# Optimization experiments

Hardware: AMD Instinct MI355X
Metric: run time of the kernel (lower is better)

Reference implementation:

```python
import jax, jax.numpy as jnp
import numpy as np

EMBED_DIM = 768
N_HEADS = 12
HEAD_DIM = EMBED_DIM // N_HEADS
B, T = 2, 4096


def setup_inputs() -> dict:
    key = jax.random.key(0)
    k1, k2, k3, k4, k5 = jax.random.split(key, 5)
    s = 1.0 / np.sqrt(EMBED_DIM)
    return {
        "x": jax.random.normal(k1, (B, T, EMBED_DIM), dtype=jnp.float32),
        "Wqkv": jax.random.normal(k2, (EMBED_DIM, 3 * EMBED_DIM), dtype=jnp.float32) * s,
        "bqkv": jnp.zeros((3 * EMBED_DIM,), dtype=jnp.float32),
        "Wproj": jax.random.normal(k3, (EMBED_DIM, EMBED_DIM), dtype=jnp.float32) * s,
        "bproj": jnp.zeros((EMBED_DIM,), dtype=jnp.float32),
    }


def reference(x, Wqkv, bqkv, Wproj, bproj):
    Bz, Tz, C = x.shape
    qkv = x @ Wqkv + bqkv                         # [B,T,3C]
    q, k, v = jnp.split(qkv, 3, axis=2)
    # [B,T,H,D] -> [B,H,T,D]
    def heads(t):
        return t.reshape(Bz, Tz, N_HEADS, HEAD_DIM).transpose(0, 2, 1, 3)
    q, k, v = heads(q), heads(k), heads(v)
    scale = 1.0 / np.sqrt(HEAD_DIM)
    att = jnp.einsum("bhqd,bhkd->bhqk", q, k) * scale   # [B,H,T,T]
    causal = jnp.tril(jnp.ones((Tz, Tz), dtype=bool))
    att = jnp.where(causal[None, None], att, -jnp.inf)
    att = jax.nn.softmax(att, axis=-1)
    y = jnp.einsum("bhqk,bhkd->bhqd", att, v)            # [B,H,T,D]
    y = y.transpose(0, 2, 1, 3).reshape(Bz, Tz, C)
    return y @ Wproj + bproj
```

## Files before the change

### kernel.cpp

```cpp
#include <hip/hip_runtime.h>
#include <math.h>
#include <stdint.h>

typedef __attribute__((ext_vector_type(8))) short bf16x8;
typedef __attribute__((ext_vector_type(4))) float f32x4;

__device__ __forceinline__ unsigned short f2bf(float f) {
    union { float f; unsigned u; } v; v.f = f;
    return (unsigned short)((v.u + 0x7fffu + ((v.u >> 16) & 1u)) >> 16);
}

__device__ __forceinline__ void gld_lds16(const void* g, void* l) {
    __builtin_amdgcn_global_load_lds(
        (const __attribute__((address_space(1))) unsigned*)(uintptr_t)g,
        (__attribute__((address_space(3))) unsigned*)(uintptr_t)l, 16, 0, 0);
}

__global__ void k_convert(const float* __restrict__ in, unsigned short* __restrict__ out, int n4) {
    int i = blockIdx.x * blockDim.x + threadIdx.x;
    if (i >= n4) return;
    float4 f = ((const float4*)in)[i];
    ushort4 o;
    o.x = f2bf(f.x); o.y = f2bf(f.y); o.z = f2bf(f.z); o.w = f2bf(f.w);
    ((ushort4*)out)[i] = o;
}

__global__ void k_transpose(const float* __restrict__ in, unsigned short* __restrict__ out, int R, int C) {
    __shared__ float tile[32][33];
    int c0 = blockIdx.x * 32, r0 = blockIdx.y * 32;
    int tx = threadIdx.x, ty = threadIdx.y;
#pragma unroll
    for (int i = 0; i < 4; ++i)
        tile[ty + i * 8][tx] = in[(size_t)(r0 + ty + i * 8) * C + c0 + tx];
    __syncthreads();
#pragma unroll
    for (int i = 0; i < 4; ++i)
        out[(size_t)(c0 + ty + i * 8) * R + r0 + tx] = f2bf(tile[tx][ty + i * 8]);
}

#define LDT 32

__device__ __forceinline__ void gemm_core(
    const unsigned short* __restrict__ A, const unsigned short* __restrict__ Bt,
    int K, unsigned short* As, unsigned short* Bs, f32x4 (&acc)[4][4])
{
    const int tid  = threadIdx.x;
    const int lane = tid & 63;
    const int w    = tid >> 6;
    const int wm   = (w >> 1) * 64, wn = (w & 1) * 64;
    const int l15  = lane & 15, quad = lane >> 4;
    const int m0 = blockIdx.x * 128, n0 = blockIdx.y * 128;

    const f32x4 zero = {0.f, 0.f, 0.f, 0.f};
#pragma unroll
    for (int i = 0; i < 4; ++i)
#pragma unroll
        for (int j = 0; j < 4; ++j) acc[i][j] = zero;

    const int r0 = tid >> 2, p8 = (tid & 3) * 8;
    const unsigned short* Ag0 = A  + (size_t)(m0 + r0) * K + p8;
    const unsigned short* Ag1 = A  + (size_t)(m0 + r0 + 64) * K + p8;
    const unsigned short* Bg0 = Bt + (size_t)(n0 + r0) * K + p8;
    const unsigned short* Bg1 = Bt + (size_t)(n0 + r0 + 64) * K + p8;
    unsigned short* lA0 = As + r0 * LDT + p8;
    unsigned short* lA1 = lA0 + 64 * LDT;
    unsigned short* lB0 = Bs + r0 * LDT + p8;
    unsigned short* lB1 = lB0 + 64 * LDT;

    const int nk = K >> 5;
    for (int kt = 0; kt < nk; ++kt) {
        __syncthreads();
        gld_lds16(Ag0, lA0);
        gld_lds16(Ag1, lA1);
        gld_lds16(Bg0, lB0);
        gld_lds16(Bg1, lB1);
        Ag0 += 32; Ag1 += 32; Bg0 += 32; Bg1 += 32;
        __syncthreads();
        bf16x8 af[4], bfr[4];
#pragma unroll
        for (int mi = 0; mi < 4; ++mi)
            af[mi] = *(const bf16x8*)&As[(wm + mi * 16 + l15) * LDT + quad * 8];
#pragma unroll
        for (int nj = 0; nj < 4; ++nj)
            bfr[nj] = *(const bf16x8*)&Bs[(wn + nj * 16 + l15) * LDT + quad * 8];
#pragma unroll
        for (int mi = 0; mi < 4; ++mi)
#pragma unroll
            for (int nj = 0; nj < 4; ++nj)
                acc[mi][nj] = __builtin_amdgcn_mfma_f32_16x16x32_bf16(af[mi], bfr[nj], acc[mi][nj], 0, 0, 0);
    }
}

__global__ __launch_bounds__(256) void k_gemm_qkv(
    const unsigned short* __restrict__ A, const unsigned short* __restrict__ Bt,
    const float* __restrict__ bias,
    unsigned short* __restrict__ QL, unsigned short* __restrict__ KL,
    unsigned short* __restrict__ VL)
{
    __shared__ __align__(16) unsigned short As[128 * LDT];
    __shared__ __align__(16) unsigned short Bs[128 * LDT];
    f32x4 acc[4][4];
    gemm_core(A, Bt, 768, As, Bs, acc);

    const int tid = threadIdx.x, lane = tid & 63, w = tid >> 6;
    const int wm = (w >> 1) * 64, wn = (w & 1) * 64;
    const int l15 = lane & 15, quad = lane >> 4;
    const int m0 = blockIdx.x * 128, n0 = blockIdx.y * 128;
    const float cscale = 0.18033688011f;
#pragma unroll
    for (int nj = 0; nj < 4; ++nj) {
        int cg = n0 + wn + nj * 16 + l15;
        float bv = bias[cg];
        int which = cg / 768;
        int rem = cg - which * 768;
        int hd = rem >> 6, d = rem & 63;
        float sc = (which == 0) ? cscale : 1.0f;
#pragma unroll
        for (int mi = 0; mi < 4; ++mi) {
#pragma unroll
            for (int r = 0; r < 4; ++r) {
                int rg = m0 + wm + mi * 16 + quad * 4 + r;
                int b = rg >> 12, tk = rg & 4095;
                int bh = b * 12 + hd;
                unsigned short ob = f2bf((acc[mi][nj][r] + bv) * sc);
                if (which == 0) {
                    size_t idx = ((((size_t)bh * 128 + (tk >> 5)) * 2 + ((tk >> 4) & 1)) * 2 + (d >> 5)) * 512
                               + ((d >> 3) & 3) * 128 + (tk & 15) * 8 + (d & 7);
                    QL[idx] = ob;
                } else if (which == 1) {
                    size_t idx = ((((size_t)bh * 64 + (tk >> 6)) * 4 + ((tk >> 4) & 3)) * 2 + (d >> 5)) * 512
                               + ((d >> 3) & 3) * 128 + (tk & 15) * 8 + (d & 7);
                    KL[idx] = ob;
                } else {
                    int wi = tk & 63;
                    size_t idx = ((((size_t)bh * 64 + (tk >> 6)) * 4 + (d >> 4)) * 2 + (wi >> 5)) * 512
                               + ((wi >> 3) & 3) * 128 + (d & 15) * 8 + (wi & 7);
                    VL[idx] = ob;
                }
            }
        }
    }
}

__global__ __launch_bounds__(256) void k_gemm_proj(
    const unsigned short* __restrict__ A, const unsigned short* __restrict__ Bt,
    const float* __restrict__ bias, float* __restrict__ out)
{
    __shared__ __align__(16) unsigned short As[128 * LDT];
    __shared__ __align__(16) unsigned short Bs[128 * LDT];
    f32x4 acc[4][4];
    gemm_core(A, Bt, 768, As, Bs, acc);

    const int tid = threadIdx.x, lane = tid & 63, w = tid >> 6;
    const int wm = (w >> 1) * 64, wn = (w & 1) * 64;
    const int l15 = lane & 15, quad = lane >> 4;
    const int m0 = blockIdx.x * 128, n0 = blockIdx.y * 128;
#pragma unroll
    for (int nj = 0; nj < 4; ++nj) {
        int cg = n0 + wn + nj * 16 + l15;
        float bv = bias[cg];
#pragma unroll
        for (int mi = 0; mi < 4; ++mi)
#pragma unroll
            for (int r = 0; r < 4; ++r) {
                int rg = m0 + wm + mi * 16 + quad * 4 + r;
                out[(size_t)rg * 768 + cg] = acc[mi][nj][r] + bv;
            }
    }
}

#define LDP 68

__global__ __launch_bounds__(128) void k_attn(
    const unsigned short* __restrict__ QL, const unsigned short* __restrict__ KL,
    const unsigned short* __restrict__ VL, unsigned short* __restrict__ Y)
{
    __shared__ __align__(16) char smem[17408];
    unsigned short* Ps = (unsigned short*)smem;

    const int tid = threadIdx.x, lane = tid & 63;
    const int w = __builtin_amdgcn_readfirstlane(tid >> 6);
    const int l15 = lane & 15, quad = lane >> 4;
    const int id = blockIdx.x;
    const int bh = id % 24;
    const int g  = 63 - id / 24;
    const int qi = 2 * g + w;
    const int q0 = qi * 32;
    const int nkt = g + 1;
    unsigned short* Pw = Ps + w * 2 * 32 * LDP;

    const int pw_off = l15 * LDP + quad * 4;
    const int pr_off = l15 * LDP + quad * 8;

    const unsigned short* Qb = QL + (((size_t)bh * 128 + qi) * 4) * 512 + lane * 8;
    const unsigned short* kp = KL + ((size_t)bh * 64) * 4096 + lane * 8;
    const unsigned short* vp = VL + ((size_t)bh * 64) * 4096 + lane * 8;

    bf16x8 qt[2][2];
#pragma unroll
    for (int m = 0; m < 2; ++m)
#pragma unroll
        for (int h = 0; h < 2; ++h)
            qt[m][h] = *(const bf16x8*)(Qb + (m * 2 + h) * 512);

    const f32x4 zero = {0.f, 0.f, 0.f, 0.f};
    f32x4 O[2][4], lac[2];
#pragma unroll
    for (int m = 0; m < 2; ++m) {
        lac[m] = zero;
#pragma unroll
        for (int dj = 0; dj < 4; ++dj) O[m][dj] = zero;
    }

    const short ONE = (short)0x3F80;
    const bf16x8 onesf = {ONE, ONE, ONE, ONE, ONE, ONE, ONE, ONE};

    bf16x8 ka[4][2], vf[4][2];
#pragma unroll
    for (int i = 0; i < 4; ++i)
#pragma unroll
        for (int h = 0; h < 2; ++h)
            ka[i][h] = *(const bf16x8*)(kp + (i * 2 + h) * 512);
#pragma unroll
    for (int dj = 0; dj < 4; ++dj)
#pragma unroll
        for (int h = 0; h < 2; ++h)
            vf[dj][h] = *(const bf16x8*)(vp + (dj * 2 + h) * 512);

    {
        f32x4 st[2][4];
#pragma unroll
        for (int i = 0; i < 4; ++i)
#pragma unroll
            for (int m = 0; m < 2; ++m) {
                f32x4 z = __builtin_amdgcn_mfma_f32_16x16x32_bf16(ka[i][0], qt[m][0], zero, 0, 0, 0);
                st[m][i] = __builtin_amdgcn_mfma_f32_16x16x32_bf16(ka[i][1], qt[m][1], z, 0, 0, 0);
            }
        if (nkt == 1) {
#pragma unroll
            for (int m = 0; m < 2; ++m)
#pragma unroll
                for (int i = 0; i < 4; ++i)
#pragma unroll
                    for (int r = 0; r < 4; ++r)
                        if (i * 16 + quad * 4 + r > q0 + m * 16 + l15)
                            st[m][i][r] = -INFINITY;
        }
#pragma unroll
        for (int m = 0; m < 2; ++m)
#pragma unroll
            for (int i = 0; i < 4; ++i) {
                unsigned e0 = __float_as_uint(__builtin_amdgcn_exp2f(st[m][i][0])) + 0x8000u;
                unsigned e1 = __float_as_uint(__builtin_amdgcn_exp2f(st[m][i][1])) + 0x8000u;
                unsigned e2 = __float_as_uint(__builtin_amdgcn_exp2f(st[m][i][2])) + 0x8000u;
                unsigned e3 = __float_as_uint(__builtin_amdgcn_exp2f(st[m][i][3])) + 0x8000u;
                uint2 pk;
                pk.x = __builtin_amdgcn_perm(e1, e0, 0x07060302);
                pk.y = __builtin_amdgcn_perm(e3, e2, 0x07060302);
                *(uint2*)(Pw + pw_off + m * 16 * LDP + i * 16) = pk;
            }
    }

    for (int kt = 0; kt < nkt; ++kt) {
        unsigned short* bc = Pw + (kt & 1) * 32 * LDP;
        unsigned short* bn = Pw + ((kt & 1) ^ 1) * 32 * LDP;
        const bool more = (kt + 1 < nkt);

        bf16x8 pa[2][2];
#pragma unroll
        for (int m = 0; m < 2; ++m) {
            pa[m][0] = *(const bf16x8*)(bc + pr_off + m * 16 * LDP);
            pa[m][1] = *(const bf16x8*)(bc + pr_off + m * 16 * LDP + 32);
        }

        if (more) {
            kp += 4096;
#pragma unroll
            for (int i = 0; i < 4; ++i)
#pragma unroll
                for (int h = 0; h < 2; ++h)
                    ka[i][h] = *(const bf16x8*)(kp + (i * 2 + h) * 512);
        }

        __builtin_amdgcn_s_setprio(1);
#pragma unroll
        for (int m = 0; m < 2; ++m) {
            f32x4 z = __builtin_amdgcn_mfma_f32_16x16x32_bf16(pa[m][0], onesf, lac[m], 0, 0, 0);
            lac[m] = __builtin_amdgcn_mfma_f32_16x16x32_bf16(pa[m][1], onesf, z, 0, 0, 0);
        }
#pragma unroll
        for (int dj = 0; dj < 4; ++dj)
#pragma unroll
            for (int m = 0; m < 2; ++m) {
                f32x4 z = __builtin_amdgcn_mfma_f32_16x16x32_bf16(pa[m][0], vf[dj][0], O[m][dj], 0, 0, 0);
                O[m][dj] = __builtin_amdgcn_mfma_f32_16x16x32_bf16(pa[m][1], vf[dj][1], z, 0, 0, 0);
            }
        __builtin_amdgcn_s_setprio(0);

        if (more) {
            vp += 4096;
#pragma unroll
            for (int dj = 0; dj < 4; ++dj)
#pragma unroll
                for (int h = 0; h < 2; ++h)
                    vf[dj][h] = *(const bf16x8*)(vp + (dj * 2 + h) * 512);

            __builtin_amdgcn_s_setprio(1);
            f32x4 st[2][4];
#pragma unroll
            for (int i = 0; i < 4; ++i)
#pragma unroll
                for (int m = 0; m < 2; ++m) {
                    f32x4 z = __builtin_amdgcn_mfma_f32_16x16x32_bf16(ka[i][0], qt[m][0], zero, 0, 0, 0);
                    st[m][i] = __builtin_amdgcn_mfma_f32_16x16x32_bf16(ka[i][1], qt[m][1], z, 0, 0, 0);
                }
            __builtin_amdgcn_s_setprio(0);
            if (kt + 1 == nkt - 1) {
                const int kb = (kt + 1) * 64;
#pragma unroll
                for (int m = 0; m < 2; ++m)
#pragma unroll
                    for (int i = 0; i < 4; ++i)
#pragma unroll
                        for (int r = 0; r < 4; ++r)
                            if (kb + i * 16 + quad * 4 + r > q0 + m * 16 + l15)
                                st[m][i][r] = -INFINITY;
            }
#pragma unroll
            for (int m = 0; m < 2; ++m)
#pragma unroll
                for (int i = 0; i < 4; ++i) {
                    unsigned e0 = __float_as_uint(__builtin_amdgcn_exp2f(st[m][i][0])) + 0x8000u;
                    unsigned e1 = __float_as_uint(__builtin_amdgcn_exp2f(st[m][i][1])) + 0x8000u;
                    unsigned e2 = __float_as_uint(__builtin_amdgcn_exp2f(st[m][i][2])) + 0x8000u;
                    unsigned e3 = __float_as_uint(__builtin_amdgcn_exp2f(st[m][i][3])) + 0x8000u;
                    uint2 pk;
                    pk.x = __builtin_amdgcn_perm(e1, e0, 0x07060302);
                    pk.y = __builtin_amdgcn_perm(e3, e2, 0x07060302);
                    *(uint2*)(bn + pw_off + m * 16 * LDP + i * 16) = pk;
                }
        }
    }

    const int b = bh / 12, hd = bh % 12;
#pragma unroll
    for (int m = 0; m < 2; ++m)
#pragma unroll
        for (int r = 0; r < 4; ++r) {
            float inv = 1.0f / lac[m][r];
            int t = q0 + 16 * m + quad * 4 + r;
            size_t base = ((size_t)(b * 4096 + t)) * 768 + hd * 64;
#pragma unroll
            for (int dj = 0; dj < 4; ++dj)
                Y[base + dj * 16 + l15] = f2bf(O[m][dj][r] * inv);
        }
}

extern "C" void kernel_launch(void* const* d_in, const int* in_sizes, int n_in,
                              void* d_out, int out_size, void* d_ws, size_t ws_size,
                              hipStream_t stream) {
    (void)in_sizes; (void)n_in; (void)out_size; (void)ws_size;
    const float* x     = (const float*)d_in[0];
    const float* Wqkv  = (const float*)d_in[1];
    const float* bqkv  = (const float*)d_in[2];
    const float* Wproj = (const float*)d_in[3];
    const float* bproj = (const float*)d_in[4];
    float* out = (float*)d_out;

    char* ws = (char*)d_ws;
    size_t off = 0;
    auto alloc = [&](size_t bytes) -> void* {
        void* p = ws + off;
        off += (bytes + 255) & ~(size_t)255;
        return p;
    };
    unsigned short* xb     = (unsigned short*)alloc((size_t)8192 * 768 * 2);
    unsigned short* WqkvT  = (unsigned short*)alloc((size_t)2304 * 768 * 2);
    unsigned short* WprojT = (unsigned short*)alloc((size_t)768 * 768 * 2);
    unsigned short* QLb    = (unsigned short*)alloc((size_t)24 * 4096 * 64 * 2);
    unsigned short* KLb    = (unsigned short*)alloc((size_t)24 * 4096 * 64 * 2);
    unsigned short* VLb    = (unsigned short*)alloc((size_t)24 * 4096 * 64 * 2);
    unsigned short* Yb     = (unsigned short*)alloc((size_t)8192 * 768 * 2);

    k_convert<<<6144, 256, 0, stream>>>(x, xb, 8192 * 768 / 4);
    dim3 tb(32, 8);
    k_transpose<<<dim3(72, 24), tb, 0, stream>>>(Wqkv, WqkvT, 768, 2304);
    k_transpose<<<dim3(24, 24), tb, 0, stream>>>(Wproj, WprojT, 768, 768);
    k_gemm_qkv<<<dim3(64, 18), 256, 0, stream>>>(xb, WqkvT, bqkv, QLb, KLb, VLb);
    k_attn<<<dim3(1536), 128, 0, stream>>>(QLb, KLb, VLb, Yb);
    k_gemm_proj<<<dim3(64, 6), 256, 0, stream>>>(Yb, WprojT, bproj, out);
}
```

Before: 246.2 us.

## Process 64 query rows per single-wave attention block to reuse K/V fragments

The attention kernel changes from two waves of 32 query rows each to one wave covering all 64 query rows of the block. Each K/V fragment loaded from global memory is now reused across four 16-row query tiles instead of two, which halves redundant K/V loads per query. In exchange, blocks are 64 threads with doubled accumulator and Q register state per wave, so register pressure rises and fewer waves are available to hide latency. The S and P work is also interleaved per 16-row group.

```diff
diff --git a/kernel.cpp b/kernel.cpp
--- a/kernel.cpp
+++ b/kernel.cpp
@@ -171,42 +171,38 @@
 
 #define LDP 68
 
-__global__ __launch_bounds__(128) void k_attn(
+__global__ __launch_bounds__(64) void k_attn(
     const unsigned short* __restrict__ QL, const unsigned short* __restrict__ KL,
     const unsigned short* __restrict__ VL, unsigned short* __restrict__ Y)
 {
-    __shared__ __align__(16) char smem[17408];
-    unsigned short* Ps = (unsigned short*)smem;
-
-    const int tid = threadIdx.x, lane = tid & 63;
-    const int w = __builtin_amdgcn_readfirstlane(tid >> 6);
+    __shared__ __align__(16) unsigned short Ps[2 * 64 * LDP];
+
+    const int lane = threadIdx.x & 63;
     const int l15 = lane & 15, quad = lane >> 4;
     const int id = blockIdx.x;
     const int bh = id % 24;
     const int g  = 63 - id / 24;
-    const int qi = 2 * g + w;
-    const int q0 = qi * 32;
+    const int q0 = g * 64;
     const int nkt = g + 1;
-    unsigned short* Pw = Ps + w * 2 * 32 * LDP;
 
     const int pw_off = l15 * LDP + quad * 4;
     const int pr_off = l15 * LDP + quad * 8;
 
-    const unsigned short* Qb = QL + (((size_t)bh * 128 + qi) * 4) * 512 + lane * 8;
+    const unsigned short* Qb = QL + (((size_t)bh * 128 + 2 * g) * 4) * 512 + lane * 8;
     const unsigned short* kp = KL + ((size_t)bh * 64) * 4096 + lane * 8;
     const unsigned short* vp = VL + ((size_t)bh * 64) * 4096 + lane * 8;
 
-    bf16x8 qt[2][2];
-#pragma unroll
-    for (int m = 0; m < 2; ++m)
+    bf16x8 qt[4][2];
+#pragma unroll
+    for (int m = 0; m < 4; ++m)
 #pragma unroll
         for (int h = 0; h < 2; ++h)
-            qt[m][h] = *(const bf16x8*)(Qb + (m * 2 + h) * 512);
+            qt[m][h] = *(const bf16x8*)(Qb + ((m >> 1) * 4 + (m & 1) * 2 + h) * 512);
 
     const f32x4 zero = {0.f, 0.f, 0.f, 0.f};
-    f32x4 O[2][4], lac[2];
-#pragma unroll
-    for (int m = 0; m < 2; ++m) {
+    f32x4 O[4][4], lac[4];
+#pragma unroll
+    for (int m = 0; m < 4; ++m) {
         lac[m] = zero;
 #pragma unroll
         for (int dj = 0; dj < 4; ++dj) O[m][dj] = zero;
@@ -227,51 +223,39 @@
         for (int h = 0; h < 2; ++h)
             vf[dj][h] = *(const bf16x8*)(vp + (dj * 2 + h) * 512);
 
-    {
-        f32x4 st[2][4];
-#pragma unroll
-        for (int i = 0; i < 4; ++i)
-#pragma unroll
-            for (int m = 0; m < 2; ++m) {
-                f32x4 z = __builtin_amdgcn_mfma_f32_16x16x32_bf16(ka[i][0], qt[m][0], zero, 0, 0, 0);
-                st[m][i] = __builtin_amdgcn_mfma_f32_16x16x32_bf16(ka[i][1], qt[m][1], z, 0, 0, 0);
-            }
+#pragma unroll
+    for (int m = 0; m < 4; ++m) {
+        f32x4 st[4];
+#pragma unroll
+        for (int i = 0; i < 4; ++i) {
+            f32x4 z = __builtin_amdgcn_mfma_f32_16x16x32_bf16(ka[i][0], qt[m][0], zero, 0, 0, 0);
+            st[i] = __builtin_amdgcn_mfma_f32_16x16x32_bf16(ka[i][1], qt[m][1], z, 0, 0, 0);
+        }
         if (nkt == 1) {
 #pragma unroll
-            for (int m = 0; m < 2; ++m)
-#pragma unroll
-                for (int i = 0; i < 4; ++i)
-#pragma unroll
-                    for (int r = 0; r < 4; ++r)
-                        if (i * 16 + quad * 4 + r > q0 + m * 16 + l15)
-                            st[m][i][r] = -INFINITY;
-        }
-#pragma unroll
-        for (int m = 0; m < 2; ++m)
-#pragma unroll
-            for (int i = 0; i < 4; ++i) {
-                unsigned e0 = __float_as_uint(__builtin_amdgcn_exp2f(st[m][i][0])) + 0x8000u;
-                unsigned e1 = __float_as_uint(__builtin_amdgcn_exp2f(st[m][i][1])) + 0x8000u;
-                unsigned e2 = __float_as_uint(__builtin_amdgcn_exp2f(st[m][i][2])) + 0x8000u;
-                unsigned e3 = __float_as_uint(__builtin_amdgcn_exp2f(st[m][i][3])) + 0x8000u;
-                uint2 pk;
-                pk.x = __builtin_amdgcn_perm(e1, e0, 0x07060302);
-                pk.y = __builtin_amdgcn_perm(e3, e2, 0x07060302);
-                *(uint2*)(Pw + pw_off + m * 16 * LDP + i * 16) = pk;
-            }
+            for (int i = 0; i < 4; ++i)
+#pragma unroll
+                for (int r = 0; r < 4; ++r)
+                    if (i * 16 + quad * 4 + r > q0 + m * 16 + l15)
+                        st[i][r] = -INFINITY;
+        }
+#pragma unroll
+        for (int i = 0; i < 4; ++i) {
+            unsigned e0 = __float_as_uint(__builtin_amdgcn_exp2f(st[i][0])) + 0x8000u;
+            unsigned e1 = __float_as_uint(__builtin_amdgcn_exp2f(st[i][1])) + 0x8000u;
+            unsigned e2 = __float_as_uint(__builtin_amdgcn_exp2f(st[i][2])) + 0x8000u;
+            unsigned e3 = __float_as_uint(__builtin_amdgcn_exp2f(st[i][3])) + 0x8000u;
+            uint2 pk;
+            pk.x = __builtin_amdgcn_perm(e1, e0, 0x07060302);
+            pk.y = __builtin_amdgcn_perm(e3, e2, 0x07060302);
+            *(uint2*)(Ps + pw_off + m * 16 * LDP + i * 16) = pk;
+        }
     }
 
     for (int kt = 0; kt < nkt; ++kt) {
-        unsigned short* bc = Pw + (kt & 1) * 32 * LDP;
-        unsigned short* bn = Pw + ((kt & 1) ^ 1) * 32 * LDP;
+        unsigned short* bc = Ps + (kt & 1) * 64 * LDP;
+        unsigned short* bn = Ps + ((kt & 1) ^ 1) * 64 * LDP;
         const bool more = (kt + 1 < nkt);
-
-        bf16x8 pa[2][2];
-#pragma unroll
-        for (int m = 0; m < 2; ++m) {
-            pa[m][0] = *(const bf16x8*)(bc + pr_off + m * 16 * LDP);
-            pa[m][1] = *(const bf16x8*)(bc + pr_off + m * 16 * LDP + 32);
-        }
 
         if (more) {
             kp += 4096;
@@ -284,17 +268,17 @@
 
         __builtin_amdgcn_s_setprio(1);
 #pragma unroll
-        for (int m = 0; m < 2; ++m) {
-            f32x4 z = __builtin_amdgcn_mfma_f32_16x16x32_bf16(pa[m][0], onesf, lac[m], 0, 0, 0);
-            lac[m] = __builtin_amdgcn_mfma_f32_16x16x32_bf16(pa[m][1], onesf, z, 0, 0, 0);
-        }
-#pragma unroll
-        for (int dj = 0; dj < 4; ++dj)
-#pragma unroll
-            for (int m = 0; m < 2; ++m) {
-                f32x4 z = __builtin_amdgcn_mfma_f32_16x16x32_bf16(pa[m][0], vf[dj][0], O[m][dj], 0, 0, 0);
-                O[m][dj] = __builtin_amdgcn_mfma_f32_16x16x32_bf16(pa[m][1], vf[dj][1], z, 0, 0, 0);
+        for (int m = 0; m < 4; ++m) {
+            bf16x8 pa0 = *(const bf16x8*)(bc + pr_off + m * 16 * LDP);
+            bf16x8 pa1 = *(const bf16x8*)(bc + pr_off + m * 16 * LDP + 32);
+            f32x4 z = __builtin_amdgcn_mfma_f32_16x16x32_bf16(pa0, onesf, lac[m], 0, 0, 0);
+            lac[m] = __builtin_amdgcn_mfma_f32_16x16x32_bf16(pa1, onesf, z, 0, 0, 0);
+#pragma unroll
+            for (int dj = 0; dj < 4; ++dj) {
+                f32x4 y = __builtin_amdgcn_mfma_f32_16x16x32_bf16(pa0, vf[dj][0], O[m][dj], 0, 0, 0);
+                O[m][dj] = __builtin_amdgcn_mfma_f32_16x16x32_bf16(pa1, vf[dj][1], y, 0, 0, 0);
             }
+        }
         __builtin_amdgcn_s_setprio(0);
 
         if (more) {
@@ -305,46 +289,44 @@
                 for (int h = 0; h < 2; ++h)
                     vf[dj][h] = *(const bf16x8*)(vp + (dj * 2 + h) * 512);
 
-            __builtin_amdgcn_s_setprio(1);
-            f32x4 st[2][4];
-#pragma unroll
-            for (int i = 0; i < 4; ++i)
-#pragma unroll
-                for (int m = 0; m < 2; ++m) {
+            const int kb = (kt + 1) * 64;
+            const bool diag = (kt + 1 == nkt - 1);
+#pragma unroll
+            for (int m = 0; m < 4; ++m) {
+                __builtin_amdgcn_s_setprio(1);
+                f32x4 st[4];
+#pragma unroll
+                for (int i = 0; i < 4; ++i) {
                     f32x4 z = __builtin_amdgcn_mfma_f32_16x16x32_bf16(ka[i][0], qt[m][0], zero, 0, 0, 0);
-                    st[m][i] = __builtin_amdgcn_mfma_f32_16x16x32_bf16(ka[i][1], qt[m][1], z, 0, 0, 0);
+                    st[i] = __builtin_amdgcn_mfma_f32_16x16x32_bf16(ka[i][1], qt[m][1], z, 0, 0, 0);
                 }
-            __builtin_amdgcn_s_setprio(0);
-            if (kt + 1 == nkt - 1) {
-                const int kb = (kt + 1) * 64;
-#pragma unroll
-                for (int m = 0; m < 2; ++m)
+                __builtin_amdgcn_s_setprio(0);
+                if (diag) {
 #pragma unroll
                     for (int i = 0; i < 4; ++i)
 #pragma unroll
                         for (int r = 0; r < 4; ++r)
                             if (kb + i * 16 + quad * 4 + r > q0 + m * 16 + l15)
-                                st[m][i][r] = -INFINITY;
-            }
-#pragma unroll
-            for (int m = 0; m < 2; ++m)
+                                st[i][r] = -INFINITY;
+                }
 #pragma unroll
                 for (int i = 0; i < 4; ++i) {
-                    unsigned e0 = __float_as_uint(__builtin_amdgcn_exp2f(st[m][i][0])) + 0x8000u;
-                    unsigned e1 = __float_as_uint(__builtin_amdgcn_exp2f(st[m][i][1])) + 0x8000u;
-                    unsigned e2 = __float_as_uint(__builtin_amdgcn_exp2f(st[m][i][2])) + 0x8000u;
-                    unsigned e3 = __float_as_uint(__builtin_amdgcn_exp2f(st[m][i][3])) + 0x8000u;
+                    unsigned e0 = __float_as_uint(__builtin_amdgcn_exp2f(st[i][0])) + 0x8000u;
+                    unsigned e1 = __float_as_uint(__builtin_amdgcn_exp2f(st[i][1])) + 0x8000u;
+                    unsigned e2 = __float_as_uint(__builtin_amdgcn_exp2f(st[i][2])) + 0x8000u;
+                    unsigned e3 = __float_as_uint(__builtin_amdgcn_exp2f(st[i][3])) + 0x8000u;
                     uint2 pk;
                     pk.x = __builtin_amdgcn_perm(e1, e0, 0x07060302);
                     pk.y = __builtin_amdgcn_perm(e3, e2, 0x07060302);
                     *(uint2*)(bn + pw_off + m * 16 * LDP + i * 16) = pk;
                 }
+            }
         }
     }
 
     const int b = bh / 12, hd = bh % 12;
 #pragma unroll
-    for (int m = 0; m < 2; ++m)
+    for (int m = 0; m < 4; ++m)
 #pragma unroll
         for (int r = 0; r < 4; ++r) {
             float inv = 1.0f / lac[m][r];
@@ -387,6 +369,6 @@
     k_transpose<<<dim3(72, 24), tb, 0, stream>>>(Wqkv, WqkvT, 768, 2304);
     k_transpose<<<dim3(24, 24), tb, 0, stream>>>(Wproj, WprojT, 768, 768);
     k_gemm_qkv<<<dim3(64, 18), 256, 0, stream>>>(xb, WqkvT, bqkv, QLb, KLb, VLb);
-    k_attn<<<dim3(1536), 128, 0, stream>>>(QLb, KLb, VLb, Yb);
+    k_attn<<<dim3(1536), 64, 0, stream>>>(QLb, KLb, VLb, Yb);
     k_gemm_proj<<<dim3(64, 6), 256, 0, stream>>>(Yb, WprojT, bproj, out);
 }
```

Result: slower. 282.9 us (+14.9%).

## Share K/V tiles across four waves via LDS with async global-to-LDS prefetch

Applied to the files above, without the earlier changes.

The attention kernel now runs 4 waves per block, each handling one 32-row query tile. K and V tiles are staged once per block into double-buffered LDS with global_load_lds prefetch, replacing the per-wave direct global loads into registers. Each wave stops at its own causal diagonal, while the block-wide loop runs to the longest wave's length and syncs every iteration. This cuts redundant global/L2 traffic for K/V at the cost of a barrier per tile, idle waves on the shorter query tiles, and larger LDS use per block.

```diff
diff --git a/kernel.cpp b/kernel.cpp
--- a/kernel.cpp
+++ b/kernel.cpp
@@ -171,30 +171,33 @@
 
 #define LDP 68
 
-__global__ __launch_bounds__(128) void k_attn(
+__global__ __launch_bounds__(256) void k_attn(
     const unsigned short* __restrict__ QL, const unsigned short* __restrict__ KL,
     const unsigned short* __restrict__ VL, unsigned short* __restrict__ Y)
 {
-    __shared__ __align__(16) char smem[17408];
-    unsigned short* Ps = (unsigned short*)smem;
+    __shared__ __align__(16) unsigned short Kb[2 * 4096];
+    __shared__ __align__(16) unsigned short Vb[2 * 4096];
+    __shared__ __align__(16) unsigned short Ps[4 * 2 * 32 * LDP];
 
     const int tid = threadIdx.x, lane = tid & 63;
     const int w = __builtin_amdgcn_readfirstlane(tid >> 6);
     const int l15 = lane & 15, quad = lane >> 4;
     const int id = blockIdx.x;
     const int bh = id % 24;
-    const int g  = 63 - id / 24;
-    const int qi = 2 * g + w;
+    const int gi = 31 - id / 24;
+    const int qi = 4 * gi + w;
     const int q0 = qi * 32;
-    const int nkt = g + 1;
-    unsigned short* Pw = Ps + w * 2 * 32 * LDP;
+    const int nkt = 2 * gi + 2;
+    const int ktd = qi >> 1;
+    const int nw  = ktd + 1;
+    unsigned short* Pw = Ps + w * (2 * 32 * LDP);
 
     const int pw_off = l15 * LDP + quad * 4;
     const int pr_off = l15 * LDP + quad * 8;
 
     const unsigned short* Qb = QL + (((size_t)bh * 128 + qi) * 4) * 512 + lane * 8;
-    const unsigned short* kp = KL + ((size_t)bh * 64) * 4096 + lane * 8;
-    const unsigned short* vp = VL + ((size_t)bh * 64) * 4096 + lane * 8;
+    const unsigned short* Kg = KL + ((size_t)bh * 64) * 4096;
+    const unsigned short* Vg = VL + ((size_t)bh * 64) * 4096;
 
     bf16x8 qt[2][2];
 #pragma unroll
@@ -211,23 +214,26 @@
 #pragma unroll
         for (int dj = 0; dj < 4; ++dj) O[m][dj] = zero;
     }
-
     const short ONE = (short)0x3F80;
     const bf16x8 onesf = {ONE, ONE, ONE, ONE, ONE, ONE, ONE, ONE};
 
-    bf16x8 ka[4][2], vf[4][2];
-#pragma unroll
-    for (int i = 0; i < 4; ++i)
-#pragma unroll
-        for (int h = 0; h < 2; ++h)
-            ka[i][h] = *(const bf16x8*)(kp + (i * 2 + h) * 512);
-#pragma unroll
-    for (int dj = 0; dj < 4; ++dj)
-#pragma unroll
-        for (int h = 0; h < 2; ++h)
-            vf[dj][h] = *(const bf16x8*)(vp + (dj * 2 + h) * 512);
+    gld_lds16(Kg + tid * 8,            Kb + tid * 8);
+    gld_lds16(Kg + 2048 + tid * 8,     Kb + 2048 + tid * 8);
+    gld_lds16(Kg + 4096 + tid * 8,     Kb + 4096 + tid * 8);
+    gld_lds16(Kg + 6144 + tid * 8,     Kb + 6144 + tid * 8);
+    gld_lds16(Vg + tid * 8,            Vb + tid * 8);
+    gld_lds16(Vg + 2048 + tid * 8,     Vb + 2048 + tid * 8);
+    __syncthreads();
 
     {
+        bf16x8 ka[4][2];
+#pragma unroll
+        for (int i = 0; i < 4; ++i)
+#pragma unroll
+            for (int h = 0; h < 2; ++h)
+                ka[i][h] = *(const bf16x8*)(Kb + (i * 2 + h) * 512 + lane * 8);
+        __syncthreads();
+
         f32x4 st[2][4];
 #pragma unroll
         for (int i = 0; i < 4; ++i)
@@ -236,7 +242,7 @@
                 f32x4 z = __builtin_amdgcn_mfma_f32_16x16x32_bf16(ka[i][0], qt[m][0], zero, 0, 0, 0);
                 st[m][i] = __builtin_amdgcn_mfma_f32_16x16x32_bf16(ka[i][1], qt[m][1], z, 0, 0, 0);
             }
-        if (nkt == 1) {
+        if (ktd == 0) {
 #pragma unroll
             for (int m = 0; m < 2; ++m)
 #pragma unroll
@@ -262,48 +268,59 @@
     }
 
     for (int kt = 0; kt < nkt; ++kt) {
-        unsigned short* bc = Pw + (kt & 1) * 32 * LDP;
-        unsigned short* bn = Pw + ((kt & 1) ^ 1) * 32 * LDP;
-        const bool more = (kt + 1 < nkt);
-
-        bf16x8 pa[2][2];
-#pragma unroll
-        for (int m = 0; m < 2; ++m) {
-            pa[m][0] = *(const bf16x8*)(bc + pr_off + m * 16 * LDP);
-            pa[m][1] = *(const bf16x8*)(bc + pr_off + m * 16 * LDP + 32);
-        }
-
-        if (more) {
-            kp += 4096;
+        const int cur = kt & 1;
+
+        if (kt + 2 < nkt) {
+            const unsigned short* s = Kg + (size_t)(kt + 2) * 4096;
+            unsigned short* d = Kb + cur * 4096;
+            gld_lds16(s + tid * 8, d + tid * 8);
+            gld_lds16(s + 2048 + tid * 8, d + 2048 + tid * 8);
+        }
+        if (kt + 1 < nkt) {
+            const unsigned short* s = Vg + (size_t)(kt + 1) * 4096;
+            unsigned short* d = Vb + (cur ^ 1) * 4096;
+            gld_lds16(s + tid * 8, d + tid * 8);
+            gld_lds16(s + 2048 + tid * 8, d + 2048 + tid * 8);
+        }
+
+        if (kt < nw) {
+            const unsigned short* bc = Pw + cur * 32 * LDP;
+            bf16x8 pa[2][2];
+#pragma unroll
+            for (int m = 0; m < 2; ++m) {
+                pa[m][0] = *(const bf16x8*)(bc + pr_off + m * 16 * LDP);
+                pa[m][1] = *(const bf16x8*)(bc + pr_off + m * 16 * LDP + 32);
+            }
+            bf16x8 vf[4][2];
+#pragma unroll
+            for (int dj = 0; dj < 4; ++dj)
+#pragma unroll
+                for (int h = 0; h < 2; ++h)
+                    vf[dj][h] = *(const bf16x8*)(Vb + cur * 4096 + (dj * 2 + h) * 512 + lane * 8);
+
+            __builtin_amdgcn_s_setprio(1);
+#pragma unroll
+            for (int m = 0; m < 2; ++m) {
+                f32x4 z = __builtin_amdgcn_mfma_f32_16x16x32_bf16(pa[m][0], onesf, lac[m], 0, 0, 0);
+                lac[m] = __builtin_amdgcn_mfma_f32_16x16x32_bf16(pa[m][1], onesf, z, 0, 0, 0);
+            }
+#pragma unroll
+            for (int dj = 0; dj < 4; ++dj)
+#pragma unroll
+                for (int m = 0; m < 2; ++m) {
+                    f32x4 y = __builtin_amdgcn_mfma_f32_16x16x32_bf16(pa[m][0], vf[dj][0], O[m][dj], 0, 0, 0);
+                    O[m][dj] = __builtin_amdgcn_mfma_f32_16x16x32_bf16(pa[m][1], vf[dj][1], y, 0, 0, 0);
+                }
+            __builtin_amdgcn_s_setprio(0);
+        }
+
+        if (kt + 1 < nw) {
+            bf16x8 ka[4][2];
 #pragma unroll
             for (int i = 0; i < 4; ++i)
 #pragma unroll
                 for (int h = 0; h < 2; ++h)
-                    ka[i][h] = *(const bf16x8*)(kp + (i * 2 + h) * 512);
-        }
-
-        __builtin_amdgcn_s_setprio(1);
-#pragma unroll
-        for (int m = 0; m < 2; ++m) {
-            f32x4 z = __builtin_amdgcn_mfma_f32_16x16x32_bf16(pa[m][0], onesf, lac[m], 0, 0, 0);
-            lac[m] = __builtin_amdgcn_mfma_f32_16x16x32_bf16(pa[m][1], onesf, z, 0, 0, 0);
-        }
-#pragma unroll
-        for (int dj = 0; dj < 4; ++dj)
-#pragma unroll
-            for (int m = 0; m < 2; ++m) {
-                f32x4 z = __builtin_amdgcn_mfma_f32_16x16x32_bf16(pa[m][0], vf[dj][0], O[m][dj], 0, 0, 0);
-                O[m][dj] = __builtin_amdgcn_mfma_f32_16x16x32_bf16(pa[m][1], vf[dj][1], z, 0, 0, 0);
-            }
-        __builtin_amdgcn_s_setprio(0);
-
-        if (more) {
-            vp += 4096;
-#pragma unroll
-            for (int dj = 0; dj < 4; ++dj)
-#pragma unroll
-                for (int h = 0; h < 2; ++h)
-                    vf[dj][h] = *(const bf16x8*)(vp + (dj * 2 + h) * 512);
+                    ka[i][h] = *(const bf16x8*)(Kb + (cur ^ 1) * 4096 + (i * 2 + h) * 512 + lane * 8);
 
             __builtin_amdgcn_s_setprio(1);
             f32x4 st[2][4];
@@ -315,7 +332,7 @@
                     st[m][i] = __builtin_amdgcn_mfma_f32_16x16x32_bf16(ka[i][1], qt[m][1], z, 0, 0, 0);
                 }
             __builtin_amdgcn_s_setprio(0);
-            if (kt + 1 == nkt - 1) {
+            if (kt + 1 == ktd) {
                 const int kb = (kt + 1) * 64;
 #pragma unroll
                 for (int m = 0; m < 2; ++m)
@@ -326,6 +343,7 @@
                             if (kb + i * 16 + quad * 4 + r > q0 + m * 16 + l15)
                                 st[m][i][r] = -INFINITY;
             }
+            unsigned short* bn = Pw + (cur ^ 1) * 32 * LDP;
 #pragma unroll
             for (int m = 0; m < 2; ++m)
 #pragma unroll
@@ -340,6 +358,8 @@
                     *(uint2*)(bn + pw_off + m * 16 * LDP + i * 16) = pk;
                 }
         }
+
+        __syncthreads();
     }
 
     const int b = bh / 12, hd = bh % 12;
@@ -387,6 +407,6 @@
     k_transpose<<<dim3(72, 24), tb, 0, stream>>>(Wqkv, WqkvT, 768, 2304);
     k_transpose<<<dim3(24, 24), tb, 0, stream>>>(Wproj, WprojT, 768, 768);
     k_gemm_qkv<<<dim3(64, 18), 256, 0, stream>>>(xb, WqkvT, bqkv, QLb, KLb, VLb);
-    k_attn<<<dim3(1536), 128, 0, stream>>>(QLb, KLb, VLb, Yb);
+    k_attn<<<dim3(768), 256, 0, stream>>>(QLb, KLb, VLb, Yb);
     k_gemm_proj<<<dim3(64, 6), 256, 0, stream>>>(Yb, WprojT, bproj, out);
 }
```

Measured after the change: 288.2 us. +17.1%, slower.
